# Kernel tuning notes

Hardware: AMD Instinct MI355X
Metric: run time of the kernel (lower is better)

The kernel has to match this reference:

```python
import jax, jax.numpy as jnp
import numpy as np

IOU_TR = 0.3
SCORE_TR = 0.1
EPS = 1e-9
N_DET = 4096
N_CLASSES = 20


def setup_inputs() -> dict:
    key = jax.random.key(0)
    k1, k2, k3, k4 = jax.random.split(key, 4)
    scores = jax.random.uniform(k1, (N_DET,), dtype=jnp.float32)
    classes = jax.random.randint(k2, (N_DET,), 0, N_CLASSES).astype(jnp.float32)
    centers = jax.random.uniform(k3, (N_DET, 3), dtype=jnp.float32) * 64.0
    dims = jax.random.uniform(k4, (N_DET, 3), dtype=jnp.float32) * 8.0 + 1.0
    results = jnp.concatenate([scores[:, None], classes[:, None], centers, dims], axis=1)
    return {"results": results}


def _pairwise_iou3d(boxes):
    # boxes: [N, 6] = (cx, cy, cz, w, h, d) center format
    c = boxes[:, :3]
    d = boxes[:, 3:]
    lo = c - d * 0.5  # [N,3]
    hi = c + d * 0.5
    inter_lo = jnp.maximum(lo[:, None, :], lo[None, :, :])  # [N,N,3]
    inter_hi = jnp.minimum(hi[:, None, :], hi[None, :, :])
    inter = jnp.prod(jnp.clip(inter_hi - inter_lo, 0.0, None), axis=-1)  # [N,N]
    vol = jnp.prod(d, axis=-1)  # [N]
    union = vol[:, None] + vol[None, :] - inter
    return inter / (union + EPS)


def reference(results):
    # results: [N, 8] = (score, class, cx, cy, cz, w, h, d)
    N = results.shape[0]
    order = jnp.argsort(-results[:, 0])  # sort by score descending
    r = results[order]
    valid = r[:, 0] >= SCORE_TR  # score threshold filter
    iou = _pairwise_iou3d(r[:, 2:])  # [N,N]
    idx = jnp.arange(N)

    def body(i, state):
        keep, active = state
        cur = active[i]
        keep = keep.at[i].set(cur)
        # suppress later boxes whose IoU with box i exceeds threshold
        sup = cur & (iou[i] > IOU_TR) & (idx > i)
        active = active & (~sup)
        return keep, active

    keep, _ = jax.lax.fori_loop(0, N, body, (jnp.zeros(N, dtype=bool), valid))
    # static-shape output: suppressed / filtered rows zeroed instead of compacted
    return jnp.where(keep[:, None], r, jnp.zeros_like(r))
```

## Files before the change

kernel.cpp:

```cpp
#include <hip/hip_runtime.h>

typedef unsigned long long u64;

#define N_DET 4096
#define NW 64
#define IOU_TR 0.3f
#define SCORE_TR 0.1f
#define EPS 1e-9f


__device__ __forceinline__ u64 rl64(u64 v, int l) {
    unsigned lo = __builtin_amdgcn_readlane((unsigned)v, l);
    unsigned hi = __builtin_amdgcn_readlane((unsigned)(v >> 32), l);
    return ((u64)hi << 32) | lo;
}

__global__ void __launch_bounds__(256) k_sort(const float* __restrict__ res,
                                              float* __restrict__ rows,
                                              float* __restrict__ soa,
                                              u64* __restrict__ A) {
    __shared__ float s[N_DET];
    int tid = threadIdx.x;
    if (blockIdx.x == 0 && tid < 64) A[tid] = 0ull;
    for (int j = tid; j < N_DET; j += 256) s[j] = res[j * 8];
    __syncthreads();
    int r = tid >> 4, c = tid & 15;
    int gi = blockIdx.x * 16 + r;
    float sc = s[gi];
    int part = 0;
    int j0 = c * 256;
    for (int j = j0; j < j0 + 256; ++j) {
        float sj = s[j];
        part += (sj > sc) || (sj == sc && j < gi);
    }
    part += __shfl_xor(part, 1, 64);
    part += __shfl_xor(part, 2, 64);
    part += __shfl_xor(part, 4, 64);
    part += __shfl_xor(part, 8, 64);
    if (c == 0) {
        int rank = part;
        float4 a = *(const float4*)(res + gi * 8);
        float4 b = *(const float4*)(res + gi * 8 + 4);
        *(float4*)(rows + rank * 8)     = a;
        *(float4*)(rows + rank * 8 + 4) = b;
        float cx = a.z, cy = a.w, cz = b.x, dx = b.y, dy = b.z, dz = b.w;
        soa[0 * N_DET + rank] = cx - dx * 0.5f;
        soa[1 * N_DET + rank] = cy - dy * 0.5f;
        soa[2 * N_DET + rank] = cz - dz * 0.5f;
        soa[3 * N_DET + rank] = cx + dx * 0.5f;
        soa[4 * N_DET + rank] = cy + dy * 0.5f;
        soa[5 * N_DET + rank] = cz + dz * 0.5f;
        soa[6 * N_DET + rank] = (dx * dy) * dz;
    }
}

__global__ void k_sup(const float* __restrict__ soa, u64* __restrict__ Trm,
                      u64* __restrict__ A) {
    int lane = threadIdx.x & 63;
    int wave = threadIdx.x >> 6;
    int i = blockIdx.x * 4 + wave;
    float ilox = soa[0 * N_DET + i], iloy = soa[1 * N_DET + i], iloz = soa[2 * N_DET + i];
    float ihix = soa[3 * N_DET + i], ihiy = soa[4 * N_DET + i], ihiz = soa[5 * N_DET + i];
    float ivol = soa[6 * N_DET + i];
    u64 rowword = 0, rowOr = 0;
    for (int w = (i >> 6); w < NW; ++w) {
        int j = w * 64 + lane;
        float lox = soa[0 * N_DET + j], loy = soa[1 * N_DET + j], loz = soa[2 * N_DET + j];
        float hix = soa[3 * N_DET + j], hiy = soa[4 * N_DET + j], hiz = soa[5 * N_DET + j];
        float vol = soa[6 * N_DET + j];
        float ix = fminf(ihix, hix) - fmaxf(ilox, lox); ix = fmaxf(ix, 0.0f);
        float iy = fminf(ihiy, hiy) - fmaxf(iloy, loy); iy = fmaxf(iy, 0.0f);
        float iz = fminf(ihiz, hiz) - fmaxf(iloz, loz); iz = fmaxf(iz, 0.0f);
        float inter = (ix * iy) * iz;
        float uni = ivol + vol - inter;
        float iou = inter / (uni + EPS);
        bool sb = (iou > IOU_TR) && (j > i);
        u64 m = __ballot(sb);
        rowOr |= m;
        rowword = (lane == w) ? m : rowword;
    }
    if (rowOr) {
        Trm[(size_t)i * NW + lane] = rowword;
        if (lane == 0) atomicOr(&A[i >> 6], 1ull << (i & 63));
    }
}

#define FIDX(V, GB) { V = (unsigned)s_nlist[(GB) + (lane & 15)]; }

#define IS1(V, P, S) { unsigned si_ = __builtin_amdgcn_readlane((V), (S)); \
    P##S = Trm[(size_t)si_ * NW + lane]; }

#define IS16(V, P) IS1(V,P,0) IS1(V,P,1) IS1(V,P,2) IS1(V,P,3)   \
    IS1(V,P,4) IS1(V,P,5) IS1(V,P,6) IS1(V,P,7)                  \
    IS1(V,P,8) IS1(V,P,9) IS1(V,P,10) IS1(V,P,11)                \
    IS1(V,P,12) IS1(V,P,13) IS1(V,P,14) IS1(V,P,15)

#define PR1(V, P, S) { unsigned si_ = __builtin_amdgcn_readlane((V), (S)); \
    u64 awd_ = rl64(act, (int)(si_ >> 6));                                 \
    u64 bit_ = (awd_ >> (si_ & 63u)) & 1ull;                               \
    u64 m_ = (0ull - bit_) & (0ull - (u64)(si_ != 4095u));                 \
    act &= ~(P##S & m_); }

#define PR16(V, P) PR1(V,P,0) PR1(V,P,1) PR1(V,P,2) PR1(V,P,3)   \
    PR1(V,P,4) PR1(V,P,5) PR1(V,P,6) PR1(V,P,7)                  \
    PR1(V,P,8) PR1(V,P,9) PR1(V,P,10) PR1(V,P,11)                \
    PR1(V,P,12) PR1(V,P,13) PR1(V,P,14) PR1(V,P,15)

__global__ void __launch_bounds__(256, 1)
k_scan(const u64* __restrict__ Trm, const u64* __restrict__ A,
       const float* __restrict__ rows, u64* __restrict__ keep) {
    __shared__ u64 s_valid[NW];
    __shared__ unsigned short s_nlist[4224];
    const int tid = threadIdx.x;
    const int wv = tid >> 6;
    const int lane = tid & 63;

    for (int w = wv * 16; w < wv * 16 + 16; ++w) {
        float scw = rows[(w * 64 + lane) * 8];
        u64 m = __ballot(scw >= SCORE_TR);
        if (lane == 0) s_valid[w] = m;
    }
    __syncthreads();
    if (wv != 0) return;

    u64 act = s_valid[lane];
    u64 avA = A[lane];
    int pc = __popcll(avA);
    int inc = pc;
#pragma unroll
    for (int d = 1; d < 64; d <<= 1) {
        int t = __shfl_up(inc, d, 64);
        if (lane >= d) inc += t;
    }
    int exc = inc - pc;
    int nTotal = __shfl(inc, 63, 64);
    {
        u64 m = avA; int o = exc;
        while (m) {
            int k = __builtin_ctzll(m); m &= m - 1;
            s_nlist[o++] = (unsigned short)(lane * 64 + k);
        }
    }
    int padded = (nTotal + 63) & ~63;
    for (int t = nTotal + lane; t < padded + 128; t += 64)
        s_nlist[t] = (unsigned short)4095;
    __threadfence_block();

    if (padded > 0) {
        u64 pa0,pa1,pa2,pa3,pa4,pa5,pa6,pa7,
            pa8,pa9,pa10,pa11,pa12,pa13,pa14,pa15;
        u64 pb0,pb1,pb2,pb3,pb4,pb5,pb6,pb7,
            pb8,pb9,pb10,pb11,pb12,pb13,pb14,pb15;
        unsigned iA0, iA1, iB0, iB1;
        FIDX(iA0, 0)  IS16(iA0, pa)
        FIDX(iB0, 16) IS16(iB0, pb)
        int g = 0;
        while (g < padded) {
            FIDX(iA1, g + 32)
            PR16(iA0, pa)
            IS16(iA1, pa)
            FIDX(iB1, g + 48)
            PR16(iB0, pb)
            IS16(iB1, pb)
            g += 32;
            if (g >= padded) break;
            FIDX(iA0, g + 32)
            PR16(iA1, pa)
            IS16(iA0, pa)
            FIDX(iB0, g + 48)
            PR16(iB1, pb)
            IS16(iB0, pb)
            g += 32;
        }
    }
    keep[lane] = act;
}

__global__ void k_out(const float* __restrict__ rows,
                      const u64* __restrict__ keep,
                      float* __restrict__ out) {
    int i = blockIdx.x * 256 + threadIdx.x;
    bool kp = (keep[i >> 6] >> (i & 63)) & 1ull;
    float4 a = kp ? ((const float4*)rows)[i * 2]     : make_float4(0.f, 0.f, 0.f, 0.f);
    float4 b = kp ? ((const float4*)rows)[i * 2 + 1] : make_float4(0.f, 0.f, 0.f, 0.f);
    ((float4*)out)[i * 2]     = a;
    ((float4*)out)[i * 2 + 1] = b;
}

extern "C" void kernel_launch(void* const* d_in, const int* in_sizes, int n_in,
                              void* d_out, int out_size, void* d_ws, size_t ws_size,
                              hipStream_t stream) {
    const float* res = (const float*)d_in[0];
    float* out = (float*)d_out;

    float* rows = (float*)d_ws;
    float* soa  = rows + N_DET * 8;
    u64* A      = (u64*)(soa + 7 * N_DET);
    u64* keep   = A + NW;
    u64* Trm    = keep + NW;

    k_sort<<<N_DET / 16, 256, 0, stream>>>(res, rows, soa, A);
    k_sup <<<N_DET / 4, 256, 0, stream>>>(soa, Trm, A);
    k_scan<<<1, 256, 0, stream>>>(Trm, A, rows, keep);
    k_out <<<16, 256, 0, stream>>>(rows, keep, out);
}
```

Baseline: 59.38 us.

## Process two boxes per wave in IoU kernel and cache active word in scan

```diff
diff --git a/kernel.cpp b/kernel.cpp
--- a/kernel.cpp
+++ b/kernel.cpp
@@ -1,6 +1,8 @@
 #include <hip/hip_runtime.h>
 
 typedef unsigned long long u64;
+typedef unsigned int u32;
+typedef unsigned short u16;
 
 #define N_DET 4096
 #define NW 64
@@ -58,36 +60,50 @@
                       u64* __restrict__ A) {
     int lane = threadIdx.x & 63;
     int wave = threadIdx.x >> 6;
-    int i = blockIdx.x * 4 + wave;
-    float ilox = soa[0 * N_DET + i], iloy = soa[1 * N_DET + i], iloz = soa[2 * N_DET + i];
-    float ihix = soa[3 * N_DET + i], ihiy = soa[4 * N_DET + i], ihiz = soa[5 * N_DET + i];
-    float ivol = soa[6 * N_DET + i];
-    u64 rowword = 0, rowOr = 0;
-    for (int w = (i >> 6); w < NW; ++w) {
+    int p = blockIdx.x * 4 + wave;
+    int i0 = 2 * p, i1 = i0 + 1;
+    float alx = soa[0*N_DET+i0], aly = soa[1*N_DET+i0], alz = soa[2*N_DET+i0];
+    float ahx = soa[3*N_DET+i0], ahy = soa[4*N_DET+i0], ahz = soa[5*N_DET+i0];
+    float av  = soa[6*N_DET+i0];
+    float blx = soa[0*N_DET+i1], bly = soa[1*N_DET+i1], blz = soa[2*N_DET+i1];
+    float bhx = soa[3*N_DET+i1], bhy = soa[4*N_DET+i1], bhz = soa[5*N_DET+i1];
+    float bv  = soa[6*N_DET+i1];
+    u64 rw0 = 0, rw1 = 0, or0 = 0, or1 = 0;
+    for (int w = (i0 >> 6); w < NW; ++w) {
         int j = w * 64 + lane;
-        float lox = soa[0 * N_DET + j], loy = soa[1 * N_DET + j], loz = soa[2 * N_DET + j];
-        float hix = soa[3 * N_DET + j], hiy = soa[4 * N_DET + j], hiz = soa[5 * N_DET + j];
-        float vol = soa[6 * N_DET + j];
-        float ix = fminf(ihix, hix) - fmaxf(ilox, lox); ix = fmaxf(ix, 0.0f);
-        float iy = fminf(ihiy, hiy) - fmaxf(iloy, loy); iy = fmaxf(iy, 0.0f);
-        float iz = fminf(ihiz, hiz) - fmaxf(iloz, loz); iz = fmaxf(iz, 0.0f);
-        float inter = (ix * iy) * iz;
-        float uni = ivol + vol - inter;
-        float iou = inter / (uni + EPS);
-        bool sb = (iou > IOU_TR) && (j > i);
-        u64 m = __ballot(sb);
-        rowOr |= m;
-        rowword = (lane == w) ? m : rowword;
-    }
-    if (rowOr) {
-        Trm[(size_t)i * NW + lane] = rowword;
-        if (lane == 0) atomicOr(&A[i >> 6], 1ull << (i & 63));
-    }
-}
-
-#define FIDX(V, GB) { V = (unsigned)s_nlist[(GB) + (lane & 15)]; }
-
-#define IS1(V, P, S) { unsigned si_ = __builtin_amdgcn_readlane((V), (S)); \
+        float lox = soa[0*N_DET+j], loy = soa[1*N_DET+j], loz = soa[2*N_DET+j];
+        float hix = soa[3*N_DET+j], hiy = soa[4*N_DET+j], hiz = soa[5*N_DET+j];
+        float vol = soa[6*N_DET+j];
+        float ix = fminf(ahx,hix)-fmaxf(alx,lox); ix = fmaxf(ix,0.f);
+        float iy = fminf(ahy,hiy)-fmaxf(aly,loy); iy = fmaxf(iy,0.f);
+        float iz = fminf(ahz,hiz)-fmaxf(alz,loz); iz = fmaxf(iz,0.f);
+        float in0 = (ix * iy) * iz;
+        float un0 = av + vol - in0;
+        float q0 = in0 / (un0 + EPS);
+        u64 m0 = __ballot(q0 > IOU_TR && j > i0);
+        float jx = fminf(bhx,hix)-fmaxf(blx,lox); jx = fmaxf(jx,0.f);
+        float jy = fminf(bhy,hiy)-fmaxf(bly,loy); jy = fmaxf(jy,0.f);
+        float jz = fminf(bhz,hiz)-fmaxf(blz,loz); jz = fmaxf(jz,0.f);
+        float in1 = (jx * jy) * jz;
+        float un1 = bv + vol - in1;
+        float q1 = in1 / (un1 + EPS);
+        u64 m1 = __ballot(q1 > IOU_TR && j > i1);
+        or0 |= m0; rw0 = (lane == w) ? m0 : rw0;
+        or1 |= m1; rw1 = (lane == w) ? m1 : rw1;
+    }
+    if (or0) {
+        Trm[(size_t)i0 * NW + lane] = rw0;
+        if (lane == 0) atomicOr(&A[i0 >> 6], 1ull << (i0 & 63));
+    }
+    if (or1) {
+        Trm[(size_t)i1 * NW + lane] = rw1;
+        if (lane == 0) atomicOr(&A[i1 >> 6], 1ull << (i1 & 63));
+    }
+}
+
+#define FIDX(V, GB) { V = (u32)s_nlist[(GB) + (lane & 15)]; }
+
+#define IS1(V, P, S) { u32 si_ = (u32)__builtin_amdgcn_readlane((V), (S)); \
     P##S = Trm[(size_t)si_ * NW + lane]; }
 
 #define IS16(V, P) IS1(V,P,0) IS1(V,P,1) IS1(V,P,2) IS1(V,P,3)   \
@@ -95,11 +111,14 @@
     IS1(V,P,8) IS1(V,P,9) IS1(V,P,10) IS1(V,P,11)                \
     IS1(V,P,12) IS1(V,P,13) IS1(V,P,14) IS1(V,P,15)
 
-#define PR1(V, P, S) { unsigned si_ = __builtin_amdgcn_readlane((V), (S)); \
-    u64 awd_ = rl64(act, (int)(si_ >> 6));                                 \
-    u64 bit_ = (awd_ >> (si_ & 63u)) & 1ull;                               \
-    u64 m_ = (0ull - bit_) & (0ull - (u64)(si_ != 4095u));                 \
-    act &= ~(P##S & m_); }
+#define PR1(V, P, S) { \
+    u32 si_ = (u32)__builtin_amdgcn_readlane((V), (S)); \
+    u32 w_ = si_ >> 6; \
+    if (w_ != s_w) {                        \
+        s_cur = rl64(act, (int)w_); s_w = w_; } \
+    if (si_ != 4095u && ((s_cur >> (si_ & 63u)) & 1ull)) {   \
+        act &= ~P##S;                       \
+        s_cur &= ~rl64(P##S, (int)w_);      } }
 
 #define PR16(V, P) PR1(V,P,0) PR1(V,P,1) PR1(V,P,2) PR1(V,P,3)   \
     PR1(V,P,4) PR1(V,P,5) PR1(V,P,6) PR1(V,P,7)                  \
@@ -110,7 +129,7 @@
 k_scan(const u64* __restrict__ Trm, const u64* __restrict__ A,
        const float* __restrict__ rows, u64* __restrict__ keep) {
     __shared__ u64 s_valid[NW];
-    __shared__ unsigned short s_nlist[4224];
+    __shared__ u16 s_nlist[4224];
     const int tid = threadIdx.x;
     const int wv = tid >> 6;
     const int lane = tid & 63;
@@ -138,12 +157,12 @@
         u64 m = avA; int o = exc;
         while (m) {
             int k = __builtin_ctzll(m); m &= m - 1;
-            s_nlist[o++] = (unsigned short)(lane * 64 + k);
+            s_nlist[o++] = (u16)(lane * 64 + k);
         }
     }
     int padded = (nTotal + 63) & ~63;
     for (int t = nTotal + lane; t < padded + 128; t += 64)
-        s_nlist[t] = (unsigned short)4095;
+        s_nlist[t] = (u16)4095;
     __threadfence_block();
 
     if (padded > 0) {
@@ -151,7 +170,9 @@
             pa8,pa9,pa10,pa11,pa12,pa13,pa14,pa15;
         u64 pb0,pb1,pb2,pb3,pb4,pb5,pb6,pb7,
             pb8,pb9,pb10,pb11,pb12,pb13,pb14,pb15;
-        unsigned iA0, iA1, iB0, iB1;
+        u32 iA0, iA1, iB0, iB1;
+        u32 s_w = 0xFFFFFFFFu;
+        u64 s_cur = 0ull;
         FIDX(iA0, 0)  IS16(iA0, pa)
         FIDX(iB0, 16) IS16(iB0, pb)
         int g = 0;
@@ -200,7 +221,7 @@
     u64* Trm    = keep + NW;
 
     k_sort<<<N_DET / 16, 256, 0, stream>>>(res, rows, soa, A);
-    k_sup <<<N_DET / 4, 256, 0, stream>>>(soa, Trm, A);
+    k_sup <<<512, 256, 0, stream>>>(soa, Trm, A);
     k_scan<<<1, 256, 0, stream>>>(Trm, A, rows, keep);
     k_out <<<16, 256, 0, stream>>>(rows, keep, out);
 }
```

Result: slower. 65.46 us (+10.2%).
